# Optimization experiments

Measured on AMD Instinct MI355X. Metric: run time of the kernel, lower is better.

## Reference

```python
import jax, jax.numpy as jnp
import numpy as np

L, N, E = 2048, 8, 1024
H = 16
KP = 256
KSZ = L // KP  # conv kernel size and stride = 8


def setup_inputs() -> dict:
    key = jax.random.key(0)
    ks = jax.random.split(key, 10)
    s = 0.02
    return {
        "query": jax.random.normal(ks[0], (L, N, E), jnp.float32),
        "key": jax.random.normal(ks[1], (L, N, E), jnp.float32),
        "value": jax.random.normal(ks[2], (L, N, E), jnp.float32),
        "in_proj_w": jax.random.normal(ks[3], (3 * E, E), jnp.float32) * s,
        "in_proj_b": jnp.zeros((3 * E,), jnp.float32),
        "e_w": jax.random.normal(ks[4], (E, E, KSZ), jnp.float32) * s,  # Conv1d OIH
        "e_b": jnp.zeros((E,), jnp.float32),
        "f_w": jax.random.normal(ks[5], (E, E, KSZ), jnp.float32) * s,
        "f_b": jnp.zeros((E,), jnp.float32),
        "out_w": jax.random.normal(ks[6], (E, E), jnp.float32) * s,
        "out_b": jnp.zeros((E,), jnp.float32),
    }


def _compress(x, w, b):
    # x: (S, N, E) -> conv1d over seq with kernel=stride=KSZ -> (Kp, N, E)
    xc = jnp.transpose(x, (1, 2, 0))  # (N, E, S)
    y = jax.lax.conv_general_dilated(
        xc, w, window_strides=(KSZ,), padding="VALID",
        dimension_numbers=("NCH", "OIH", "NCH"))
    y = y + b[None, :, None]
    return jnp.transpose(y, (2, 0, 1))  # (Kp, N, E)


def reference(query, key, value, in_proj_w, in_proj_b, e_w, e_b, f_w, f_b, out_w, out_b):
    D = E // H
    scaling = D ** -0.5
    q = query @ in_proj_w[:E].T + in_proj_b[:E]
    k = key @ in_proj_w[E:2 * E].T + in_proj_b[E:2 * E]
    v = value @ in_proj_w[2 * E:].T + in_proj_b[2 * E:]
    q = q * scaling
    k = _compress(k, e_w, e_b)  # (Kp, N, E)
    v = _compress(v, f_w, f_b)
    Kp = k.shape[0]
    # reshape to (N*H, len, D)
    qh = jnp.transpose(q.reshape(L, N * H, D), (1, 0, 2))
    kh = jnp.transpose(k.reshape(Kp, N * H, D), (1, 0, 2))
    vh = jnp.transpose(v.reshape(Kp, N * H, D), (1, 0, 2))
    attn = jax.nn.softmax(jnp.einsum("bld,bkd->blk", qh, kh), axis=-1)
    out = jnp.einsum("blk,bkd->bld", attn, vh)  # (N*H, L, D)
    out = jnp.transpose(out, (1, 0, 2)).reshape(L, N, E)
    out = out @ out_w.T + out_b
    attn_weights = attn.reshape(N, H, L, Kp).mean(axis=1)  # need_weights avg over heads
    return out, attn_weights
```

## Files before the change

kernel.cpp:

```cpp
#include <hip/hip_runtime.h>

typedef unsigned short u16;
typedef u16  u16x4 __attribute__((ext_vector_type(4)));
typedef u16  u16x8 __attribute__((ext_vector_type(8)));
typedef float f32x4 __attribute__((ext_vector_type(4)));
typedef int   i32x4 __attribute__((ext_vector_type(4)));
typedef __bf16 bf16x8 __attribute__((ext_vector_type(8)));

#define LSEQ 2048
#define NB 8
#define EDIM 1024
#define HNUM 16
#define DDIM 64
#define KPDIM 256
#define NE (NB*EDIM)
#define MROWS (LSEQ*NB)
#define AWSZ ((size_t)NB*LSEQ*KPDIM)

__device__ __forceinline__ u16 f2b(float f) {
  unsigned u = __builtin_bit_cast(unsigned, f);
  u += 0x7fffu + ((u >> 16) & 1u);
  return (u16)(u >> 16);
}

__device__ __forceinline__ void gl_lds16(const void* g, void* l) {
  __builtin_amdgcn_global_load_lds(
      (const __attribute__((address_space(1))) void*)g,
      (__attribute__((address_space(3))) void*)l, 16, 0, 0);
}

__device__ __forceinline__ f32x4 mfma16(bf16x8 a, bf16x8 b, f32x4 c) {
  return __builtin_amdgcn_mfma_f32_16x16x32_bf16(a, b, c, 0, 0, 0);
}

#define BAR()  __builtin_amdgcn_s_barrier()
#define WVM8() asm volatile("s_waitcnt vmcnt(8)" ::: "memory")
#define WVM0() asm volatile("s_waitcnt vmcnt(0)" ::: "memory")

__global__ void wconv(const float* __restrict__ src, u16* __restrict__ dst,
                      int n4, int scale_n4, float sc) {
  int i = blockIdx.x * blockDim.x + threadIdx.x;
  if (i >= n4) return;
  f32x4 v = ((const f32x4*)src)[i];
  float s = (i < scale_n4) ? sc : 1.0f;
  u16x4 o;
  o[0] = f2b(v[0] * s); o[1] = f2b(v[1] * s);
  o[2] = f2b(v[2] * s); o[3] = f2b(v[3] * s);
  ((u16x4*)dst)[i] = o;
}

__global__ void wtrans(const float* __restrict__ ew, const float* __restrict__ fw,
                       u16* __restrict__ eT, u16* __restrict__ fT) {
  const float* src = blockIdx.y ? fw : ew;
  u16* dst = blockIdx.y ? fT : eT;
  int eo = blockIdx.x >> 4;
  int ei0 = (blockIdx.x & 15) * 64;
  int l = threadIdx.x;
  __shared__ u16 lds[8][64];
  const float* s = src + (size_t)eo * 8192 + (size_t)ei0 * 8 + l * 8;
  f32x4 a = *(const f32x4*)s;
  f32x4 b = *(const f32x4*)(s + 4);
  float v[8] = {a[0], a[1], a[2], a[3], b[0], b[1], b[2], b[3]};
#pragma unroll
  for (int t = 0; t < 8; ++t) lds[t][l] = f2b(v[t]);
  __syncthreads();
  int t = l >> 3, c = l & 7;
  i32x4 out = *(const i32x4*)&lds[t][c * 8];
  *(i32x4*)(dst + (size_t)eo * 8192 + t * 1024 + ei0 + c * 8) = out;
}

__global__ void bscale(const float* __restrict__ b, float* __restrict__ out) {
  int i = blockIdx.x * blockDim.x + threadIdx.x;
  if (i < EDIM) out[i] = b[i] * 0.125f;
}

__global__ void castqkv(const float* __restrict__ q, const float* __restrict__ k,
                        const float* __restrict__ v, u16* __restrict__ out) {
  const float* src = blockIdx.y == 0 ? q : (blockIdx.y == 1 ? k : v);
  size_t base = (size_t)blockIdx.y * ((size_t)MROWS * EDIM);
  size_t i = ((size_t)blockIdx.x * 256 + threadIdx.x) * 8;
  f32x4 v0 = *(const f32x4*)(src + i);
  f32x4 v1 = *(const f32x4*)(src + i + 4);
  u16x8 o;
  o[0] = f2b(v0[0]); o[1] = f2b(v0[1]); o[2] = f2b(v0[2]); o[3] = f2b(v0[3]);
  o[4] = f2b(v1[0]); o[5] = f2b(v1[1]); o[6] = f2b(v1[2]); o[7] = f2b(v1[3]);
  *(u16x8*)(out + base + i) = o;
}

__global__ void redc(const float* __restrict__ part, const float* __restrict__ eb,
                     const float* __restrict__ fb, u16* __restrict__ kc,
                     u16* __restrict__ vcT) {
  int zc = blockIdx.y;
  const float* p = part + (size_t)zc * 4 * 2048 * 1024;
  const float* bias = zc ? fb : eb;
  size_t i = ((size_t)blockIdx.x * 256 + threadIdx.x) * 4;
  f32x4 s = *(const f32x4*)(p + i);
  s += *(const f32x4*)(p + 2097152 + i);
  s += *(const f32x4*)(p + 2 * 2097152 + i);
  s += *(const f32x4*)(p + 3 * 2097152 + i);
  int e = (int)(i & 1023);
  int row = (int)(i >> 10);
  int n = row >> 8, pp = row & 255;
  int h = e >> 6, d = e & 63;
  f32x4 b = *(const f32x4*)(bias + e);
  if (zc == 0) {
    u16x4 o;
    o[0] = f2b(s[0] + b[0]); o[1] = f2b(s[1] + b[1]);
    o[2] = f2b(s[2] + b[2]); o[3] = f2b(s[3] + b[3]);
    *(u16x4*)(kc + (((size_t)(n * HNUM + h) * KPDIM + pp) * DDIM + d)) = o;
  } else {
    size_t base = (size_t)(n * HNUM + h) * (DDIM * KPDIM);
#pragma unroll
    for (int q = 0; q < 4; ++q) {
      int dq = d + q;
      vcT[base + dq * 256 + (((pp >> 3) ^ (dq & 7)) * 8) + (pp & 7)] =
          f2b(s[q] + b[q]);
    }
  }
}

__global__ void awred(const float* __restrict__ awp, float* __restrict__ aw) {
  size_t i = ((size_t)blockIdx.x * 256 + threadIdx.x) * 4;
  f32x4 s = *(const f32x4*)(awp + i);
  s += *(const f32x4*)(awp + AWSZ + i);
  s += *(const f32x4*)(awp + 2 * AWSZ + i);
  s += *(const f32x4*)(awp + 3 * AWSZ + i);
  *(f32x4*)(aw + i) = s;
}

template<int AMODE, int OUTMODE>
__global__ __launch_bounds__(512, 2)
void gemm256(const void* A0p, const void* A1p, const void* A2p,
             const u16* B0p, const u16* B1p, const u16* B2p,
             const float* b0p, const float* b1p, const float* b2p,
             void* C0p, void* C1p, void* C2p,
             int M, int K, int kspl) {
  const int zc = blockIdx.z / kspl, sp = blockIdx.z % kspl;
  const void* Ap = zc == 0 ? A0p : (zc == 1 ? A1p : A2p);
  const u16* Bp = zc == 0 ? B0p : (zc == 1 ? B1p : B2p);
  const float* biasp = zc == 0 ? b0p : (zc == 1 ? b1p : b2p);
  void* Cp = zc == 0 ? C0p : (zc == 1 ? C1p : C2p);

  __shared__ u16 lds[2][2][256 * 64];

  const int tid = threadIdx.x;
  const int w = tid >> 6, lane = tid & 63;
  const int lr = lane & 15, lg = lane >> 4;
  const int wr = w >> 2, wc = w & 3;
  const int m0 = blockIdx.x * 256, n0 = blockIdx.y * 256;
  const int kper = K / kspl, kbase = sp * kper, nt = kper >> 6;

  f32x4 acc[8][4];
#pragma unroll
  for (int mi = 0; mi < 8; ++mi)
#pragma unroll
    for (int ni = 0; ni < 4; ++ni) {
      f32x4 zv = {0.f, 0.f, 0.f, 0.f};
      acc[mi][ni] = zv;
    }

  auto stage = [&](int buf, int kt) {
    const int k0 = kbase + (kt << 6);
#pragma unroll
    for (int i = 0; i < 4; ++i) {
      int c = i * 512 + tid;
      int row = c >> 3, j = c & 7, js = j ^ (row & 7);
      gl_lds16(Bp + (size_t)(n0 + row) * K + k0 + js * 8, &lds[buf][1][c * 8]);
    }
    if (AMODE == 0) {
      const u16* Ab = (const u16*)Ap;
#pragma unroll
      for (int i = 0; i < 4; ++i) {
        int c = i * 512 + tid;
        int row = c >> 3, j = c & 7, js = j ^ (row & 7);
        gl_lds16(Ab + (size_t)(m0 + row) * K + k0 + js * 8, &lds[buf][0][c * 8]);
      }
    } else {
      const u16* Ab = (const u16*)Ap;
#pragma unroll
      for (int i = 0; i < 4; ++i) {
        int c = i * 512 + tid;
        int row = c >> 3, j = c & 7, js = j ^ (row & 7);
        int m = m0 + row;
        int nn = m >> 8, p = m & 255;
        int k = k0 + js * 8;
        gl_lds16(Ab + (size_t)(p * 8 + (k >> 10)) * NE + nn * EDIM + (k & 1023),
                 &lds[buf][0][c * 8]);
      }
    }
  };

  auto LDA = [&](int buf, int row, int ks) -> bf16x8 {
    return *(const bf16x8*)&lds[buf][0][row * 64 + (((ks * 4 + lg) ^ (row & 7)) << 3)];
  };
  auto LDB = [&](int buf, int row, int ks) -> bf16x8 {
    return *(const bf16x8*)&lds[buf][1][row * 64 + (((ks * 4 + lg) ^ (row & 7)) << 3)];
  };

  stage(0, 0);
  if (nt > 1) { stage(1, 1); WVM8(); } else { WVM0(); }
  BAR();

  for (int t = 0; t < nt; ++t) {
    const int b = t & 1;
    bf16x8 a0[4][2], a1[4][2], bq0[2][2], bq1[2][2];
#pragma unroll
    for (int mi = 0; mi < 4; ++mi)
#pragma unroll
      for (int ks = 0; ks < 2; ++ks)
        a0[mi][ks] = LDA(b, wr * 128 + mi * 16 + lr, ks);
#pragma unroll
    for (int ni = 0; ni < 2; ++ni)
#pragma unroll
      for (int ks = 0; ks < 2; ++ks)
        bq0[ni][ks] = LDB(b, wc * 64 + ni * 16 + lr, ks);
    BAR();
    __builtin_amdgcn_s_setprio(1);
#pragma unroll
    for (int mi = 0; mi < 4; ++mi)
#pragma unroll
      for (int ni = 0; ni < 2; ++ni)
#pragma unroll
        for (int ks = 0; ks < 2; ++ks)
          acc[mi][ni] = mfma16(a0[mi][ks], bq0[ni][ks], acc[mi][ni]);
    __builtin_amdgcn_s_setprio(0);
    BAR();
#pragma unroll
    for (int ni = 0; ni < 2; ++ni)
#pragma unroll
      for (int ks = 0; ks < 2; ++ks)
        bq1[ni][ks] = LDB(b, wc * 64 + (ni + 2) * 16 + lr, ks);
    BAR();
    __builtin_amdgcn_s_setprio(1);
#pragma unroll
    for (int mi = 0; mi < 4; ++mi)
#pragma unroll
      for (int ni = 0; ni < 2; ++ni)
#pragma unroll
        for (int ks = 0; ks < 2; ++ks)
          acc[mi][ni + 2] = mfma16(a0[mi][ks], bq1[ni][ks], acc[mi][ni + 2]);
    __builtin_amdgcn_s_setprio(0);
    BAR();
#pragma unroll
    for (int mi = 0; mi < 4; ++mi)
#pragma unroll
      for (int ks = 0; ks < 2; ++ks)
        a1[mi][ks] = LDA(b, wr * 128 + 64 + mi * 16 + lr, ks);
    BAR();
    __builtin_amdgcn_s_setprio(1);
#pragma unroll
    for (int mi = 0; mi < 4; ++mi)
#pragma unroll
      for (int ni = 0; ni < 2; ++ni)
#pragma unroll
        for (int ks = 0; ks < 2; ++ks)
          acc[mi + 4][ni + 2] = mfma16(a1[mi][ks], bq1[ni][ks], acc[mi + 4][ni + 2]);
    __builtin_amdgcn_s_setprio(0);
    BAR();
    if (t + 2 < nt) stage(b, t + 2);
    BAR();
    __builtin_amdgcn_s_setprio(1);
#pragma unroll
    for (int mi = 0; mi < 4; ++mi)
#pragma unroll
      for (int ni = 0; ni < 2; ++ni)
#pragma unroll
        for (int ks = 0; ks < 2; ++ks)
          acc[mi + 4][ni] = mfma16(a1[mi][ks], bq0[ni][ks], acc[mi + 4][ni]);
    __builtin_amdgcn_s_setprio(0);
    if (t + 1 < nt) {
      if (t + 2 < nt) { WVM8(); } else { WVM0(); }
    }
    BAR();
  }

#pragma unroll
  for (int ni = 0; ni < 4; ++ni) {
    const int col = n0 + wc * 64 + ni * 16 + lr;
    const float bv = (OUTMODE == 2) ? 0.f : biasp[col];
#pragma unroll
    for (int mi = 0; mi < 8; ++mi)
#pragma unroll
      for (int j = 0; j < 4; ++j) {
        const int row = m0 + wr * 128 + mi * 16 + lg * 4 + j;
        const float v = acc[mi][ni][j] + bv;
        if (OUTMODE == 2)
          ((float*)Cp)[(size_t)sp * M * 1024 + (size_t)row * 1024 + col] = v;
        else if (OUTMODE == 1)
          ((float*)Cp)[(size_t)row * 1024 + col] = v;
        else
          ((u16*)Cp)[(size_t)row * 1024 + col] = f2b(v);
      }
  }
}

template<int AMODE, int OUTMODE>
__global__ __launch_bounds__(256)
void gemm_bt(const void* A0p, const void* A1p, const void* A2p,
             const u16* B0p, const u16* B1p, const u16* B2p,
             const float* b0p, const float* b1p, const float* b2p,
             void* C0p, void* C1p, void* C2p,
             int M, int K, int kspl) {
  const int zc = blockIdx.z / kspl;
  const int sp = blockIdx.z % kspl;
  const void* Ap = zc == 0 ? A0p : (zc == 1 ? A1p : A2p);
  const u16* Bp = zc == 0 ? B0p : (zc == 1 ? B1p : B2p);
  const float* biasp = zc == 0 ? b0p : (zc == 1 ? b1p : b2p);
  void* Cp = zc == 0 ? C0p : (zc == 1 ? C1p : C2p);

  __shared__ u16 Alds[128 * 64];
  __shared__ u16 Blds[128 * 64];

  const int tid = threadIdx.x;
  const int w = tid >> 6, lane = tid & 63;
  const int lr = lane & 15, lg = lane >> 4;
  const int m0 = blockIdx.x * 128, n0 = blockIdx.y * 128;
  const int wr = (w >> 1) * 64, wc = (w & 1) * 64;
  const int brow = lane >> 3;
  const int bcol = (lane & 7) * 8;

  f32x4 acc[4][4];
#pragma unroll
  for (int mi = 0; mi < 4; ++mi)
#pragma unroll
    for (int ni = 0; ni < 4; ++ni) {
      f32x4 zv = {0.f, 0.f, 0.f, 0.f};
      acc[mi][ni] = zv;
    }

  const int kper = K / kspl;
  const int ktn = kper >> 6;
  const int kb = sp * kper;
  for (int kt = 0; kt < ktn; ++kt) {
    const int k0 = kb + (kt << 6);
    __syncthreads();
#pragma unroll
    for (int i = 0; i < 4; ++i) {
      const int c = w * 4 + i;
      const int row = c * 8 + brow;
      gl_lds16(Bp + (size_t)(n0 + row) * K + k0 + bcol, &Blds[c * 512]);
    }
    if (AMODE == 2) {
      const float* Af = (const float*)Ap;
#pragma unroll
      for (int i = 0; i < 4; ++i) {
        const int c = i * 256 + tid;
        const int row = c >> 3, k8 = (c & 7) * 8;
        const float* s = Af + (size_t)(m0 + row) * K + k0 + k8;
        f32x4 v0 = *(const f32x4*)s;
        f32x4 v1 = *(const f32x4*)(s + 4);
        u16x8 pk;
        pk[0] = f2b(v0[0]); pk[1] = f2b(v0[1]); pk[2] = f2b(v0[2]); pk[3] = f2b(v0[3]);
        pk[4] = f2b(v1[0]); pk[5] = f2b(v1[1]); pk[6] = f2b(v1[2]); pk[7] = f2b(v1[3]);
        *(u16x8*)&Alds[row * 64 + k8] = pk;
      }
    } else if (AMODE == 0) {
      const u16* Ab = (const u16*)Ap;
#pragma unroll
      for (int i = 0; i < 4; ++i) {
        const int c = w * 4 + i;
        const int row = c * 8 + brow;
        gl_lds16(Ab + (size_t)(m0 + row) * K + k0 + bcol, &Alds[c * 512]);
      }
    } else {
      const u16* Ab = (const u16*)Ap;
#pragma unroll
      for (int i = 0; i < 4; ++i) {
        const int c = w * 4 + i;
        const int m = m0 + c * 8 + brow;
        const int nn = m >> 8, p = m & 255;
        const int k = k0 + bcol;
        gl_lds16(Ab + (size_t)(p * 8 + (k >> 10)) * NE + nn * EDIM + (k & 1023),
                 &Alds[c * 512]);
      }
    }
    __syncthreads();
#pragma unroll
    for (int ks = 0; ks < 2; ++ks) {
      bf16x8 af[4], bf[4];
#pragma unroll
      for (int mi = 0; mi < 4; ++mi)
        af[mi] = *(const bf16x8*)&Alds[(wr + mi * 16 + lr) * 64 + ks * 32 + lg * 8];
#pragma unroll
      for (int ni = 0; ni < 4; ++ni)
        bf[ni] = *(const bf16x8*)&Blds[(wc + ni * 16 + lr) * 64 + ks * 32 + lg * 8];
#pragma unroll
      for (int mi = 0; mi < 4; ++mi)
#pragma unroll
        for (int ni = 0; ni < 4; ++ni)
          acc[mi][ni] = mfma16(af[mi], bf[ni], acc[mi][ni]);
    }
  }
#pragma unroll
  for (int ni = 0; ni < 4; ++ni) {
    const int col = n0 + wc + ni * 16 + lr;
    const float bv = (OUTMODE == 2) ? 0.f : biasp[col];
#pragma unroll
    for (int mi = 0; mi < 4; ++mi)
#pragma unroll
      for (int j = 0; j < 4; ++j) {
        const int row = m0 + wr + mi * 16 + lg * 4 + j;
        const float v = acc[mi][ni][j] + bv;
        if (OUTMODE == 4) {
          const int nn = row >> 8, pp = row & 255, h = col >> 6, d = col & 63;
          ((u16*)Cp)[(size_t)(nn * HNUM + h) * (DDIM * KPDIM) + d * 256 +
                     (((pp >> 3) ^ (d & 7)) * 8) + (pp & 7)] = f2b(v);
        } else if (OUTMODE == 3) {
          const int nn = row >> 8, pp = row & 255, h = col >> 6, d = col & 63;
          ((u16*)Cp)[((size_t)(nn * HNUM + h) * KPDIM + pp) * DDIM + d] = f2b(v);
        } else if (OUTMODE == 2)
          ((float*)Cp)[(size_t)sp * M * 1024 + (size_t)row * 1024 + col] = v;
        else if (OUTMODE == 1)
          ((float*)Cp)[(size_t)row * 1024 + col] = v;
        else
          ((u16*)Cp)[(size_t)row * 1024 + col] = f2b(v);
      }
  }
}

__global__ __launch_bounds__(256)
void attn_fused(const u16* __restrict__ Q, const u16* __restrict__ Kc,
                const u16* __restrict__ VcT, u16* __restrict__ Aout,
                float* __restrict__ AWp, int hpg) {
  __shared__ u16 Ares[256 * 64];
  __shared__ u16 Bres[64 * 256];
  const int tid = threadIdx.x;
  const int w = tid >> 6, lane = tid & 63;
  const int lr = lane & 15, lg = lane >> 4;
  const int n = blockIdx.y;
  const int l0 = blockIdx.x * 64;
  const int lrow = l0 + w * 16 + lr;
  char* kbase = (char*)Ares;
  char* vbase = (char*)Bres;
  char* pbase = (char*)Ares + w * 8192;

  f32x4 macc[16];
#pragma unroll
  for (int ni = 0; ni < 16; ++ni) { f32x4 zv = {0.f,0.f,0.f,0.f}; macc[ni] = zv; }

  for (int hh = 0; hh < hpg; ++hh) {
    const int h = blockIdx.z * hpg + hh;
    const u16* kh = Kc + (size_t)(n * HNUM + h) * (KPDIM * DDIM);
    const u16* vh = VcT + (size_t)(n * HNUM + h) * (DDIM * KPDIM);
    __syncthreads();
#pragma unroll
    for (int it = 0; it < 8; ++it) {
      int c = it * 256 + tid;
      int p = c >> 3, j = c & 7;
      gl_lds16(kh + p * 64 + ((j ^ (p & 7)) << 3), kbase + c * 16);
    }
#pragma unroll
    for (int it = 0; it < 8; ++it) {
      int c = it * 256 + tid;
      gl_lds16(vh + c * 8, vbase + c * 16);
    }
    const u16* qp = Q + (size_t)lrow * NE + n * EDIM + h * DDIM + lg * 8;
    bf16x8 aq0 = *(const bf16x8*)qp;
    bf16x8 aq1 = *(const bf16x8*)(qp + 32);
    __syncthreads();
    f32x4 s[16];
#pragma unroll
    for (int ni = 0; ni < 16; ++ni) { f32x4 zv = {0.f,0.f,0.f,0.f}; s[ni] = zv; }
#pragma unroll
    for (int ni = 0; ni < 16; ++ni) {
      int row = ni * 16 + lr;
      const char* kr = kbase + row * 128;
      bf16x8 b0 = *(const bf16x8*)(kr + ((lg ^ (row & 7)) << 4));
      bf16x8 b1 = *(const bf16x8*)(kr + (((4 + lg) ^ (row & 7)) << 4));
      s[ni] = mfma16(aq0, b0, s[ni]);
      s[ni] = mfma16(aq1, b1, s[ni]);
    }
    float mx[4], sm[4], inv[4];
#pragma unroll
    for (int j = 0; j < 4; ++j) mx[j] = -1e30f;
#pragma unroll
    for (int ni = 0; ni < 16; ++ni)
#pragma unroll
      for (int j = 0; j < 4; ++j) mx[j] = fmaxf(mx[j], s[ni][j]);
#pragma unroll
    for (int msk = 1; msk <= 8; msk <<= 1)
#pragma unroll
      for (int j = 0; j < 4; ++j) mx[j] = fmaxf(mx[j], __shfl_xor(mx[j], msk, 64));
#pragma unroll
    for (int j = 0; j < 4; ++j) sm[j] = 0.f;
#pragma unroll
    for (int ni = 0; ni < 16; ++ni)
#pragma unroll
      for (int j = 0; j < 4; ++j) {
        float e = __expf(s[ni][j] - mx[j]);
        s[ni][j] = e; sm[j] += e;
      }
#pragma unroll
    for (int msk = 1; msk <= 8; msk <<= 1)
#pragma unroll
      for (int j = 0; j < 4; ++j) sm[j] += __shfl_xor(sm[j], msk, 64);
#pragma unroll
    for (int j = 0; j < 4; ++j) inv[j] = 1.0f / sm[j];
    __syncthreads();
#pragma unroll
    for (int ni = 0; ni < 16; ++ni)
#pragma unroll
      for (int j = 0; j < 4; ++j) {
        float pv = s[ni][j] * inv[j];
        macc[ni][j] += pv * 0.0625f;
        int r = lg * 4 + j;
        *(u16*)(pbase + r * 512 + ((ni * 32 + lr * 2) ^ ((r & 7) << 4))) = f2b(pv);
      }
    f32x4 o[4];
#pragma unroll
    for (int ni2 = 0; ni2 < 4; ++ni2) { f32x4 zv = {0.f,0.f,0.f,0.f}; o[ni2] = zv; }
#pragma unroll
    for (int ks = 0; ks < 8; ++ks) {
      bf16x8 a = *(const bf16x8*)(pbase + lr * 512 + ((ks * 64 + 16 * lg) ^ ((lr & 7) << 4)));
#pragma unroll
      for (int ni2 = 0; ni2 < 4; ++ni2) {
        int d = ni2 * 16 + lr;
        bf16x8 b = *(const bf16x8*)(vbase + d * 512 + (((ks * 4 + lg) ^ (d & 7)) << 4));
        o[ni2] = mfma16(a, b, o[ni2]);
      }
    }
#pragma unroll
    for (int ni2 = 0; ni2 < 4; ++ni2)
#pragma unroll
      for (int j = 0; j < 4; ++j) {
        int gl = l0 + w * 16 + lg * 4 + j;
        Aout[(size_t)gl * NE + n * EDIM + h * DDIM + ni2 * 16 + lr] = f2b(o[ni2][j]);
      }
  }
  float* awo = AWp + (size_t)blockIdx.z * AWSZ + (size_t)n * (LSEQ * KPDIM);
#pragma unroll
  for (int ni = 0; ni < 16; ++ni)
#pragma unroll
    for (int j = 0; j < 4; ++j) {
      int r = lg * 4 + j;
      awo[(size_t)(l0 + w * 16 + r) * KPDIM + ni * 16 + lr] = macc[ni][j];
    }
}

extern "C" void kernel_launch(void* const* d_in, const int* in_sizes, int n_in,
                              void* d_out, int out_size, void* d_ws, size_t ws_size,
                              hipStream_t stream) {
  const float* query = (const float*)d_in[0];
  const float* key   = (const float*)d_in[1];
  const float* value = (const float*)d_in[2];
  const float* ipw   = (const float*)d_in[3];
  const float* ipb   = (const float*)d_in[4];
  const float* ew    = (const float*)d_in[5];
  const float* eb    = (const float*)d_in[6];
  const float* fw    = (const float*)d_in[7];
  const float* fb    = (const float*)d_in[8];
  const float* ow    = (const float*)d_in[9];
  const float* ob    = (const float*)d_in[10];

  char* ws = (char*)d_ws;
  size_t off = 0;
  auto alloc = [&](size_t bytes) {
    void* p = ws + off;
    off += (bytes + 255) & ~(size_t)255;
    return p;
  };
  u16* qp    = (u16*)alloc((size_t)MROWS * EDIM * 2);
  u16* kp    = (u16*)alloc((size_t)MROWS * EDIM * 2);
  u16* vp    = (u16*)alloc((size_t)MROWS * EDIM * 2);
  u16* ao    = (u16*)alloc((size_t)MROWS * EDIM * 2);
  u16* kc    = (u16*)alloc((size_t)NB * KPDIM * EDIM * 2);
  u16* vcT   = (u16*)alloc((size_t)NB * KPDIM * EDIM * 2);
  u16* w_in  = (u16*)alloc((size_t)3 * EDIM * EDIM * 2);
  u16* w_eT  = (u16*)alloc((size_t)EDIM * 8 * EDIM * 2);
  u16* w_fT  = (u16*)alloc((size_t)EDIM * 8 * EDIM * 2);
  u16* w_out = (u16*)alloc((size_t)EDIM * EDIM * 2);
  float* bq  = (float*)alloc(EDIM * 4);
  size_t base_needed = off;

  size_t qkv16_b = (size_t)3 * MROWS * EDIM * 2;
  size_t part_b  = (size_t)2 * 4 * 2048 * 1024 * 4;
  bool bigX  = ws_size >= base_needed + qkv16_b;
  bool midX  = ws_size >= base_needed + part_b;
  char* X = (char*)alloc(bigX ? qkv16_b : (midX ? part_b : 0));
  u16* qkv16 = (u16*)X;
  float* part = (float*)X;
  float* awp  = (float*)X;

  float* out_f = (float*)d_out;
  float* aw_f  = (float*)d_out + (size_t)MROWS * EDIM;

  wconv<<<dim3(3072), 256, 0, stream>>>(ipw, w_in, 786432, 262144, 0.125f);
  wconv<<<dim3(1024), 256, 0, stream>>>(ow, w_out, 262144, 0, 1.0f);
  wtrans<<<dim3(16384, 2), 64, 0, stream>>>(ew, fw, w_eT, w_fT);
  bscale<<<dim3(4), 256, 0, stream>>>(ipb, bq);

  if (bigX) {
    castqkv<<<dim3(8192, 3), 256, 0, stream>>>(query, key, value, qkv16);
    gemm256<0, 0><<<dim3(64, 4, 3), 512, 0, stream>>>(
        qkv16, qkv16 + (size_t)MROWS * EDIM, qkv16 + (size_t)2 * MROWS * EDIM,
        w_in, w_in + 1048576, w_in + 2097152,
        bq, ipb + 1024, ipb + 2048,
        qp, kp, vp, MROWS, 1024, 1);
  } else {
    gemm_bt<2, 0><<<dim3(128, 8, 3), 256, 0, stream>>>(
        query, key, value,
        w_in, w_in + 1048576, w_in + 2097152,
        bq, ipb + 1024, ipb + 2048,
        qp, kp, vp, MROWS, 1024, 1);
  }

  if (bigX || midX) {
    gemm256<1, 2><<<dim3(8, 4, 8), 512, 0, stream>>>(
        kp, vp, vp,
        w_eT, w_fT, w_fT,
        eb, fb, fb,
        part, part + (size_t)4 * 2048 * 1024, part,
        NB * KPDIM, 8192, 4);
    redc<<<dim3(2048, 2), 256, 0, stream>>>(part, eb, fb, kc, vcT);
  } else {
    gemm_bt<1, 3><<<dim3(16, 8, 1), 256, 0, stream>>>(
        kp, kp, kp, w_eT, w_eT, w_eT, eb, eb, eb,
        kc, kc, kc, NB * KPDIM, 8192, 1);
    gemm_bt<1, 4><<<dim3(16, 8, 1), 256, 0, stream>>>(
        vp, vp, vp, w_fT, w_fT, w_fT, fb, fb, fb,
        vcT, vcT, vcT, NB * KPDIM, 8192, 1);
  }

  if (bigX) {
    attn_fused<<<dim3(32, 8, 4), 256, 0, stream>>>(qp, kc, vcT, ao, awp, 4);
    awred<<<dim3(4096), 256, 0, stream>>>(awp, aw_f);
  } else {
    attn_fused<<<dim3(32, 8, 1), 256, 0, stream>>>(qp, kc, vcT, ao, aw_f, 16);
  }

  gemm256<0, 1><<<dim3(64, 4, 1), 512, 0, stream>>>(
      ao, ao, ao,
      w_out, w_out, w_out,
      ob, ob, ob,
      out_f, out_f, out_f, MROWS, 1024, 1);
}
```

Measured before the change: 490.3 us.

## Stage GEMM tiles in half-tile chunks interleaved with MFMA phases and remap workgroups

Measured after the change: 451.8 us. 7.9% less time.

```diff
diff --git a/kernel.cpp b/kernel.cpp
--- a/kernel.cpp
+++ b/kernel.cpp
@@ -33,9 +33,10 @@
   return __builtin_amdgcn_mfma_f32_16x16x32_bf16(a, b, c, 0, 0, 0);
 }
 
-#define BAR()  __builtin_amdgcn_s_barrier()
-#define WVM8() asm volatile("s_waitcnt vmcnt(8)" ::: "memory")
-#define WVM0() asm volatile("s_waitcnt vmcnt(0)" ::: "memory")
+#define BAR()   __builtin_amdgcn_s_barrier()
+#define LGKM0() asm volatile("s_waitcnt lgkmcnt(0)" ::: "memory")
+#define WVM6()  asm volatile("s_waitcnt vmcnt(6)" ::: "memory")
+#define WVM0()  asm volatile("s_waitcnt vmcnt(0)" ::: "memory")
 
 __global__ void wconv(const float* __restrict__ src, u16* __restrict__ dst,
                       int n4, int scale_n4, float sc) {
@@ -135,19 +136,27 @@
              const float* b0p, const float* b1p, const float* b2p,
              void* C0p, void* C1p, void* C2p,
              int M, int K, int kspl) {
-  const int zc = blockIdx.z / kspl, sp = blockIdx.z % kspl;
+  int bid = blockIdx.x + gridDim.x * (blockIdx.y + gridDim.y * blockIdx.z);
+  const int nwg = gridDim.x * gridDim.y * gridDim.z;
+  if ((nwg & 7) == 0) bid = (bid & 7) * (nwg >> 3) + (bid >> 3);
+  const int bx = bid % gridDim.x;
+  const int rem = bid / gridDim.x;
+  const int by = rem % gridDim.y;
+  const int bz = rem / gridDim.y;
+
+  const int zc = bz / kspl, sp = bz % kspl;
   const void* Ap = zc == 0 ? A0p : (zc == 1 ? A1p : A2p);
   const u16* Bp = zc == 0 ? B0p : (zc == 1 ? B1p : B2p);
   const float* biasp = zc == 0 ? b0p : (zc == 1 ? b1p : b2p);
   void* Cp = zc == 0 ? C0p : (zc == 1 ? C1p : C2p);
 
-  __shared__ u16 lds[2][2][256 * 64];
+  __shared__ u16 lds[2][2][2][128 * 64];
 
   const int tid = threadIdx.x;
   const int w = tid >> 6, lane = tid & 63;
   const int lr = lane & 15, lg = lane >> 4;
   const int wr = w >> 2, wc = w & 3;
-  const int m0 = blockIdx.x * 256, n0 = blockIdx.y * 256;
+  const int m0 = bx * 256, n0 = by * 256;
   const int kper = K / kspl, kbase = sp * kper, nt = kper >> 6;
 
   f32x4 acc[8][4];
@@ -159,62 +168,61 @@
       acc[mi][ni] = zv;
     }
 
-  auto stage = [&](int buf, int kt) {
+  auto stage_half = [&](int buf, int op, int half, int kt) {
     const int k0 = kbase + (kt << 6);
 #pragma unroll
-    for (int i = 0; i < 4; ++i) {
+    for (int i = 0; i < 2; ++i) {
       int c = i * 512 + tid;
-      int row = c >> 3, j = c & 7, js = j ^ (row & 7);
-      gl_lds16(Bp + (size_t)(n0 + row) * K + k0 + js * 8, &lds[buf][1][c * 8]);
-    }
-    if (AMODE == 0) {
-      const u16* Ab = (const u16*)Ap;
-#pragma unroll
-      for (int i = 0; i < 4; ++i) {
-        int c = i * 512 + tid;
-        int row = c >> 3, j = c & 7, js = j ^ (row & 7);
-        gl_lds16(Ab + (size_t)(m0 + row) * K + k0 + js * 8, &lds[buf][0][c * 8]);
-      }
-    } else {
-      const u16* Ab = (const u16*)Ap;
-#pragma unroll
-      for (int i = 0; i < 4; ++i) {
-        int c = i * 512 + tid;
-        int row = c >> 3, j = c & 7, js = j ^ (row & 7);
+      int r = c >> 3, j = c & 7, js = j ^ (r & 7);
+      int row = half * 128 + r;
+      u16* dst = &lds[buf][op][half][c * 8];
+      if (op == 1) {
+        gl_lds16(Bp + (size_t)(n0 + row) * K + k0 + js * 8, dst);
+      } else if (AMODE == 0) {
+        gl_lds16((const u16*)Ap + (size_t)(m0 + row) * K + k0 + js * 8, dst);
+      } else {
         int m = m0 + row;
         int nn = m >> 8, p = m & 255;
         int k = k0 + js * 8;
-        gl_lds16(Ab + (size_t)(p * 8 + (k >> 10)) * NE + nn * EDIM + (k & 1023),
-                 &lds[buf][0][c * 8]);
+        gl_lds16((const u16*)Ap + (size_t)(p * 8 + (k >> 10)) * NE +
+                 nn * EDIM + (k & 1023), dst);
       }
     }
   };
 
   auto LDA = [&](int buf, int row, int ks) -> bf16x8 {
-    return *(const bf16x8*)&lds[buf][0][row * 64 + (((ks * 4 + lg) ^ (row & 7)) << 3)];
+    return *(const bf16x8*)&lds[buf][0][row >> 7]
+        [(row & 127) * 64 + (((ks * 4 + lg) ^ (row & 7)) << 3)];
   };
   auto LDB = [&](int buf, int row, int ks) -> bf16x8 {
-    return *(const bf16x8*)&lds[buf][1][row * 64 + (((ks * 4 + lg) ^ (row & 7)) << 3)];
+    return *(const bf16x8*)&lds[buf][1][row >> 7]
+        [(row & 127) * 64 + (((ks * 4 + lg) ^ (row & 7)) << 3)];
   };
 
-  stage(0, 0);
-  if (nt > 1) { stage(1, 1); WVM8(); } else { WVM0(); }
+  stage_half(0, 0, 0, 0); stage_half(0, 1, 0, 0);
+  stage_half(0, 1, 1, 0); stage_half(0, 0, 1, 0);
+  if (nt > 1) {
+    stage_half(1, 1, 0, 1); stage_half(1, 1, 1, 1); stage_half(1, 0, 0, 1);
+    WVM6();
+  } else {
+    WVM0();
+  }
   BAR();
 
-  for (int t = 0; t < nt; ++t) {
-    const int b = t & 1;
-    bf16x8 a0[4][2], a1[4][2], bq0[2][2], bq1[2][2];
+  for (int t = 0; t < nt; t += 2) {
+    bf16x8 a0[4][2], a1[4][2], b0f[2][2], b1f[2][2];
 #pragma unroll
     for (int mi = 0; mi < 4; ++mi)
 #pragma unroll
       for (int ks = 0; ks < 2; ++ks)
-        a0[mi][ks] = LDA(b, wr * 128 + mi * 16 + lr, ks);
+        a0[mi][ks] = LDA(0, wr * 128 + mi * 16 + lr, ks);
 #pragma unroll
     for (int ni = 0; ni < 2; ++ni)
 #pragma unroll
       for (int ks = 0; ks < 2; ++ks)
-        bq0[ni][ks] = LDB(b, wc * 64 + ni * 16 + lr, ks);
-    BAR();
+        b0f[ni][ks] = LDB(0, wc * 64 + ni * 16 + lr, ks);
+    stage_half(1, 0, 1, t + 1);
+    BAR(); LGKM0();
     __builtin_amdgcn_s_setprio(1);
 #pragma unroll
     for (int mi = 0; mi < 4; ++mi)
@@ -222,15 +230,15 @@
       for (int ni = 0; ni < 2; ++ni)
 #pragma unroll
         for (int ks = 0; ks < 2; ++ks)
-          acc[mi][ni] = mfma16(a0[mi][ks], bq0[ni][ks], acc[mi][ni]);
+          acc[mi][ni] = mfma16(a0[mi][ks], b0f[ni][ks], acc[mi][ni]);
     __builtin_amdgcn_s_setprio(0);
     BAR();
 #pragma unroll
     for (int ni = 0; ni < 2; ++ni)
 #pragma unroll
       for (int ks = 0; ks < 2; ++ks)
-        bq1[ni][ks] = LDB(b, wc * 64 + (ni + 2) * 16 + lr, ks);
-    BAR();
+        b1f[ni][ks] = LDB(0, wc * 64 + (ni + 2) * 16 + lr, ks);
+    BAR(); LGKM0();
     __builtin_amdgcn_s_setprio(1);
 #pragma unroll
     for (int mi = 0; mi < 4; ++mi)
@@ -238,15 +246,16 @@
       for (int ni = 0; ni < 2; ++ni)
 #pragma unroll
         for (int ks = 0; ks < 2; ++ks)
-          acc[mi][ni + 2] = mfma16(a0[mi][ks], bq1[ni][ks], acc[mi][ni + 2]);
+          acc[mi][ni + 2] = mfma16(a0[mi][ks], b1f[ni][ks], acc[mi][ni + 2]);
     __builtin_amdgcn_s_setprio(0);
     BAR();
 #pragma unroll
     for (int mi = 0; mi < 4; ++mi)
 #pragma unroll
       for (int ks = 0; ks < 2; ++ks)
-        a1[mi][ks] = LDA(b, wr * 128 + 64 + mi * 16 + lr, ks);
-    BAR();
+        a1[mi][ks] = LDA(0, wr * 128 + 64 + mi * 16 + lr, ks);
+    if (t + 2 < nt) stage_half(0, 1, 0, t + 2);
+    BAR(); LGKM0();
     __builtin_amdgcn_s_setprio(1);
 #pragma unroll
     for (int mi = 0; mi < 4; ++mi)
@@ -254,10 +263,10 @@
       for (int ni = 0; ni < 2; ++ni)
 #pragma unroll
         for (int ks = 0; ks < 2; ++ks)
-          acc[mi + 4][ni + 2] = mfma16(a1[mi][ks], bq1[ni][ks], acc[mi + 4][ni + 2]);
+          acc[mi + 4][ni + 2] = mfma16(a1[mi][ks], b1f[ni][ks], acc[mi + 4][ni + 2]);
     __builtin_amdgcn_s_setprio(0);
     BAR();
-    if (t + 2 < nt) stage(b, t + 2);
+    if (t + 2 < nt) { stage_half(0, 1, 1, t + 2); stage_half(0, 0, 0, t + 2); }
     BAR();
     __builtin_amdgcn_s_setprio(1);
 #pragma unroll
@@ -266,11 +275,77 @@
       for (int ni = 0; ni < 2; ++ni)
 #pragma unroll
         for (int ks = 0; ks < 2; ++ks)
-          acc[mi + 4][ni] = mfma16(a1[mi][ks], bq0[ni][ks], acc[mi + 4][ni]);
+          acc[mi + 4][ni] = mfma16(a1[mi][ks], b0f[ni][ks], acc[mi + 4][ni]);
     __builtin_amdgcn_s_setprio(0);
-    if (t + 1 < nt) {
-      if (t + 2 < nt) { WVM8(); } else { WVM0(); }
-    }
+    if (t + 2 < nt) { WVM6(); } else { WVM0(); }
+    BAR();
+#pragma unroll
+    for (int mi = 0; mi < 4; ++mi)
+#pragma unroll
+      for (int ks = 0; ks < 2; ++ks)
+        a0[mi][ks] = LDA(1, wr * 128 + mi * 16 + lr, ks);
+#pragma unroll
+    for (int ni = 0; ni < 2; ++ni)
+#pragma unroll
+      for (int ks = 0; ks < 2; ++ks)
+        b0f[ni][ks] = LDB(1, wc * 64 + ni * 16 + lr, ks);
+    if (t + 2 < nt) stage_half(0, 0, 1, t + 2);
+    BAR(); LGKM0();
+    __builtin_amdgcn_s_setprio(1);
+#pragma unroll
+    for (int mi = 0; mi < 4; ++mi)
+#pragma unroll
+      for (int ni = 0; ni < 2; ++ni)
+#pragma unroll
+        for (int ks = 0; ks < 2; ++ks)
+          acc[mi][ni] = mfma16(a0[mi][ks], b0f[ni][ks], acc[mi][ni]);
+    __builtin_amdgcn_s_setprio(0);
+    BAR();
+#pragma unroll
+    for (int ni = 0; ni < 2; ++ni)
+#pragma unroll
+      for (int ks = 0; ks < 2; ++ks)
+        b1f[ni][ks] = LDB(1, wc * 64 + (ni + 2) * 16 + lr, ks);
+    BAR(); LGKM0();
+    __builtin_amdgcn_s_setprio(1);
+#pragma unroll
+    for (int mi = 0; mi < 4; ++mi)
+#pragma unroll
+      for (int ni = 0; ni < 2; ++ni)
+#pragma unroll
+        for (int ks = 0; ks < 2; ++ks)
+          acc[mi][ni + 2] = mfma16(a0[mi][ks], b1f[ni][ks], acc[mi][ni + 2]);
+    __builtin_amdgcn_s_setprio(0);
+    BAR();
+#pragma unroll
+    for (int mi = 0; mi < 4; ++mi)
+#pragma unroll
+      for (int ks = 0; ks < 2; ++ks)
+        a1[mi][ks] = LDA(1, wr * 128 + 64 + mi * 16 + lr, ks);
+    if (t + 3 < nt) stage_half(1, 1, 0, t + 3);
+    BAR(); LGKM0();
+    __builtin_amdgcn_s_setprio(1);
+#pragma unroll
+    for (int mi = 0; mi < 4; ++mi)
+#pragma unroll
+      for (int ni = 0; ni < 2; ++ni)
+#pragma unroll
+        for (int ks = 0; ks < 2; ++ks)
+          acc[mi + 4][ni + 2] = mfma16(a1[mi][ks], b1f[ni][ks], acc[mi + 4][ni + 2]);
+    __builtin_amdgcn_s_setprio(0);
+    BAR();
+    if (t + 3 < nt) { stage_half(1, 1, 1, t + 3); stage_half(1, 0, 0, t + 3); }
+    BAR();
+    __builtin_amdgcn_s_setprio(1);
+#pragma unroll
+    for (int mi = 0; mi < 4; ++mi)
+#pragma unroll
+      for (int ni = 0; ni < 2; ++ni)
+#pragma unroll
+        for (int ks = 0; ks < 2; ++ks)
+          acc[mi + 4][ni] = mfma16(a1[mi][ks], b0f[ni][ks], acc[mi + 4][ni]);
+    __builtin_amdgcn_s_setprio(0);
+    if (t + 3 < nt) { WVM6(); } else { WVM0(); }
     BAR();
   }
 
```
